# Kernel optimization log

Measured on AMD Instinct MI355X. Metric: run time of the kernel, lower is better.

## Reference

```python
import jax, jax.numpy as jnp
import numpy as np

NUM_STATION = 20
NUM_HEADS = 8
INPUT_DIM = 128
KEY_DIM = 16          # = val_dim = embed_dim // num_heads
EMBED_DIM = 128
NORM = 1.0 / np.sqrt(KEY_DIM).astype(np.float32)


def setup_inputs() -> dict:
    key = jax.random.key(0)
    ks = jax.random.split(key, 10)
    B, N, D = 32, 1024, INPUT_DIM
    q = jax.random.normal(ks[0], (B, N, D), jnp.float32)
    h = jax.random.normal(ks[1], (B, N, D), jnp.float32)
    stdv_k = 1.0 / np.sqrt(KEY_DIM)      # torch init: uniform(-1/sqrt(last_dim), ...)
    stdv_e = 1.0 / np.sqrt(EMBED_DIM)
    def U(k, shape, s):
        return jax.random.uniform(k, shape, jnp.float32, -s, s)
    pshape = (NUM_HEADS, INPUT_DIM, KEY_DIM)
    return {
        "q": q,
        "h": h,
        "W_query_custom": U(ks[2], pshape, stdv_k),
        "W_query_custom_1": U(ks[3], pshape, stdv_k),
        "W_key_custom": U(ks[4], pshape, stdv_k),
        "W_val_custom": U(ks[5], pshape, stdv_k),
        "W_query_charge_1": U(ks[6], pshape, stdv_k),
        "W_key_charge": U(ks[7], pshape, stdv_k),
        "W_val_charge": U(ks[8], pshape, stdv_k),
        "W_out": U(ks[9], (NUM_HEADS, KEY_DIM, EMBED_DIM), stdv_e),
    }


def reference(q, h, W_query_custom, W_query_custom_1, W_key_custom, W_val_custom,
              W_query_charge_1, W_key_charge, W_val_charge, W_out):
    S = NUM_STATION + 1                      # depot + stations
    h_st, h_tk = h[:, :S], h[:, S:]          # [B,S,D], [B,T,D]
    q_st, q_tk = q[:, :S], q[:, S:]

    proj = lambda x, W: jnp.einsum('bnd,hdk->hbnk', x, W)

    K_c = proj(h_tk, W_key_custom)           # [H,B,T,K]
    V_c = proj(h_tk, W_val_custom)
    K_s = proj(h_st, W_key_charge)           # [H,B,S,K]
    V_s = proj(h_st, W_val_charge)

    # task -> task attention (queries via W_query_custom_1)
    Q_tt = proj(q_tk, W_query_custom_1)
    A_tt = jax.nn.softmax(NORM * jnp.einsum('hbqk,hbtk->hbqt', Q_tt, K_c), axis=-1)
    heads_t = jnp.einsum('hbqt,hbtk->hbqk', A_tt, V_c)

    # task -> station attention (queries via W_query_custom)
    Q_ts = proj(q_tk, W_query_custom)
    A_ts = jax.nn.softmax(NORM * jnp.einsum('hbqk,hbsk->hbqs', Q_ts, K_s), axis=-1)
    heads_t = heads_t + jnp.einsum('hbqs,hbsk->hbqk', A_ts, V_s)

    # station -> task attention (queries via W_query_charge_1)
    Q_st = proj(q_st, W_query_charge_1)
    A_st = jax.nn.softmax(NORM * jnp.einsum('hbqk,hbtk->hbqt', Q_st, K_c), axis=-1)
    heads_s = jnp.einsum('hbqt,hbtk->hbqk', A_st, V_c)

    heads = jnp.concatenate([heads_s, heads_t], axis=2)   # [H,B,N,K]
    out = jnp.einsum('hbnk,hke->bne', heads, W_out)        # [B,N,E]
    return out
```

## Files before the change

kernel.cpp:

```cpp
#include <hip/hip_runtime.h>

typedef __bf16 bf16x8 __attribute__((ext_vector_type(8)));
typedef float f32x4 __attribute__((ext_vector_type(4)));
typedef float f32x16 __attribute__((ext_vector_type(16)));
typedef unsigned int uint32;
typedef unsigned short u16;

#define NST 21
#define TOK 1003
#define SCL 0.3606737602222409f

union U4B { uint4 u; bf16x8 b; };

__device__ __forceinline__ uint32 pkbf(float a, float b) {
  uint32 ua = __float_as_uint(a), ub = __float_as_uint(b);
  ua += 0x7fffu + ((ua >> 16) & 1u);
  ub += 0x7fffu + ((ub >> 16) & 1u);
  return (ua >> 16) | (ub & 0xffff0000u);
}
__device__ __forceinline__ u16 bf1(float a) {
  uint32 u = __float_as_uint(a);
  u += 0x7fffu + ((u >> 16) & 1u);
  return (u16)(u >> 16);
}
__device__ __forceinline__ uint32 pkperm(float lo, float hi) {
  return __builtin_amdgcn_perm(__float_as_uint(hi), __float_as_uint(lo), 0x07060302u);
}
__device__ __forceinline__ void plswap(uint32& a, uint32& b) {
#if __has_builtin(__builtin_amdgcn_permlane32_swap)
  typedef unsigned int uu2 __attribute__((ext_vector_type(2)));
  uu2 r = __builtin_amdgcn_permlane32_swap(a, b, false, false);
  a = r.x; b = r.y;
#else
  asm volatile("v_permlane32_swap_b32 %0, %1" : "+v"(a), "+v"(b));
#endif
}

__global__ __launch_bounds__(256) void prep(
    const float* __restrict__ q, const float* __restrict__ hx,
    const float* __restrict__ W0, const float* __restrict__ W1,
    const float* __restrict__ W2, const float* __restrict__ W3,
    const float* __restrict__ W4, const float* __restrict__ Wqst,
    const float* __restrict__ Wks, const float* __restrict__ Wvs,
    u16* __restrict__ WtAll, u16* __restrict__ Qm,
    u16* __restrict__ Ks, u16* __restrict__ Vs) {
  int bid = blockIdx.x, tid = threadIdx.x;
  __shared__ float xq2[2][128], xh2[2][128];
  if (bid < 40) {
    int w = bid >> 3, seg = bid & 7;
    const float* W = (w == 0) ? W0 : (w == 1) ? W1 : (w == 2) ? W2
                     : (w == 3) ? W3 : W4;
    u16* dst = WtAll + w * 16384;
#pragma unroll
    for (int it = 0; it < 8; ++it) {
      int i = seg * 2048 + it * 256 + tid;
      int inner = i & 127, outer = i >> 7;
      float v;
      if (w < 4) {
        int h = outer >> 4, k = outer & 15;
        v = W[h * 2048 + inner * 16 + k];
      } else {
        v = W[inner * 128 + outer];
      }
      dst[outer * 128 + inner] = bf1(v);
    }
  } else {
    int t2 = bid - 40;
    int sub = tid >> 7, col = tid & 127;
    int hh = col >> 4, k = col & 15;
    int bs2 = t2 * 2 + sub;
    int b2 = bs2 >> 5, s = bs2 & 31;
    if (s < NST) {
      xq2[sub][col] = q[(size_t)(b2 * 1024 + s) * 128 + col];
      xh2[sub][col] = hx[(size_t)(b2 * 1024 + s) * 128 + col];
    }
    __syncthreads();
    if (s < NST) {
      const float* Wq = Wqst + hh * 2048 + k;
      const float* Wk = Wks + hh * 2048 + k;
      const float* Wv = Wvs + hh * 2048 + k;
      float dq = 0.f, dk_ = 0.f, dv = 0.f;
#pragma unroll 8
      for (int d = 0; d < 128; ++d) {
        float xq = xq2[sub][d], xh = xh2[sub][d];
        dq = fmaf(xq, Wq[d * 16], dq);
        dk_ = fmaf(xh, Wk[d * 16], dk_);
        dv = fmaf(xh, Wv[d * 16], dv);
      }
      Qm[(((size_t)hh * 32 + b2) * 1024 + s) * 16 + k] = bf1(dq * SCL);
      Ks[(((size_t)hh * 32 + b2) * 32 + s) * 16 + k] = bf1(dk_);
      Vs[(((size_t)hh * 32 + b2) * 16 + k) * 32 + s] = bf1(dv);
    } else {
      Ks[(((size_t)hh * 32 + b2) * 32 + s) * 16 + k] = 0;
      Vs[(((size_t)hh * 32 + b2) * 16 + k) * 32 + s] = 0;
    }
  }
}

__global__ __launch_bounds__(256) void proj_pair(
    const float* __restrict__ q, const float* __restrict__ hx,
    const u16* __restrict__ WtAll, u16* __restrict__ Qm,
    u16* __restrict__ Qts, u16* __restrict__ Kc, u16* __restrict__ Vc) {
  __shared__ u16 Wl[128 * 136];
  int pg = blockIdx.x >> 9, mb = blockIdx.x & 511;
  int m0 = mb * 64;
  const float* A = pg ? hx : q;
  int tid = threadIdx.x;
  int wave = tid >> 6, lane = tid & 63;
  int quad = lane >> 4, l15 = lane & 15;
  int mrow = m0 + wave * 16 + l15;

  U4B af[4];
#pragma unroll
  for (int dk = 0; dk < 4; ++dk) {
    const float* Af = A + (size_t)mrow * 128 + dk * 32 + quad * 8;
    float4 a = *(const float4*)Af;
    float4 b = *(const float4*)(Af + 4);
    af[dk].u = make_uint4(pkbf(a.x, a.y), pkbf(a.z, a.w),
                          pkbf(b.x, b.y), pkbf(b.z, b.w));
  }

  int gbase = m0 + wave * 16 + quad * 4;
  int bb = gbase >> 10, n0 = gbase & 1023;
  int token = mrow;
  int bb2 = token >> 10, tn = token & 1023;

#pragma unroll
  for (int s = 0; s < 2; ++s) {
    int mode = pg * 2 + s;
    const u16* WtG = WtAll + mode * 16384;
    if (s) __syncthreads();
#pragma unroll
    for (int r = 0; r < 8; ++r) {
      int i = r * 256 + tid;
      int e = i >> 4, j = i & 15;
      *(uint4*)&Wl[e * 136 + j * 8] = *(const uint4*)(WtG + e * 128 + j * 8);
    }
    __syncthreads();

    f32x4 c[8];
#pragma unroll
    for (int nt = 0; nt < 8; ++nt)
#pragma unroll
      for (int r = 0; r < 4; ++r) c[nt][r] = 0.f;
#pragma unroll
    for (int dk = 0; dk < 4; ++dk)
#pragma unroll
      for (int nt = 0; nt < 8; ++nt) {
        U4B bg;
        bg.u = *(const uint4*)&Wl[(nt * 16 + l15) * 136 + dk * 32 + quad * 8];
        if (mode == 3)
          c[nt] = __builtin_amdgcn_mfma_f32_16x16x32_bf16(af[dk].b, bg.b, c[nt], 0, 0, 0);
        else
          c[nt] = __builtin_amdgcn_mfma_f32_16x16x32_bf16(bg.b, af[dk].b, c[nt], 0, 0, 0);
      }

    if (mode == 3) {
#pragma unroll
      for (int nt = 0; nt < 8; ++nt) {
        uint2 w2 = make_uint2(pkbf(c[nt][0], c[nt][1]), pkbf(c[nt][2], c[nt][3]));
        *(uint2*)(Vc + (((size_t)nt * 32 + bb) * 16 + l15) * 1024 + n0) = w2;
      }
    } else {
      float scale = (mode <= 1) ? SCL : 1.0f;
      u16* dstp = (mode == 0) ? Qm : (mode == 1) ? Qts : Kc;
      if (mode != 0 || tn >= NST) {
#pragma unroll
        for (int nt = 0; nt < 8; ++nt) {
          uint2 w2 = make_uint2(pkbf(c[nt][0] * scale, c[nt][1] * scale),
                                pkbf(c[nt][2] * scale, c[nt][3] * scale));
          *(uint2*)(dstp + (((size_t)nt * 32 + bb2) * 1024 + tn) * 16 + quad * 4) = w2;
        }
      }
    }
  }
}

__global__ __launch_bounds__(256) void outproj(
    const u16* __restrict__ heads, const u16* __restrict__ WtAll,
    float* __restrict__ out) {
  __shared__ u16 Wl[128 * 136];
  const u16* WtG = WtAll + 4 * 16384;
  int tid = threadIdx.x;
#pragma unroll
  for (int r = 0; r < 8; ++r) {
    int i = r * 256 + tid;
    int e = i >> 4, j = i & 15;
    *(uint4*)&Wl[e * 136 + j * 8] = *(const uint4*)(WtG + e * 128 + j * 8);
  }
  __syncthreads();
  int wave = tid >> 6, lane = tid & 63;
  int quad = lane >> 4, l15 = lane & 15;
  int m0 = blockIdx.x * 64;
  int mrow = m0 + wave * 16 + l15;

  f32x4 c[8];
#pragma unroll
  for (int nt = 0; nt < 8; ++nt)
#pragma unroll
    for (int r = 0; r < 4; ++r) c[nt][r] = 0.f;
#pragma unroll
  for (int dk = 0; dk < 4; ++dk) {
    U4B af;
    af.u = *(const uint4*)(heads + (size_t)mrow * 128 + dk * 32 + quad * 8);
#pragma unroll
    for (int nt = 0; nt < 8; ++nt) {
      U4B bg;
      bg.u = *(const uint4*)&Wl[(nt * 16 + l15) * 136 + dk * 32 + quad * 8];
      c[nt] = __builtin_amdgcn_mfma_f32_16x16x32_bf16(bg.b, af.b, c[nt], 0, 0, 0);
    }
  }
#pragma unroll
  for (int nt = 0; nt < 8; ++nt)
    *(f32x4*)(out + (size_t)mrow * 128 + nt * 16 + quad * 4) = c[nt];
}

__global__ __launch_bounds__(256, 6) void attn_main(
    const u16* __restrict__ Qm, const u16* __restrict__ Qts,
    const u16* __restrict__ Kc, const u16* __restrict__ Vc,
    const u16* __restrict__ Ks, const u16* __restrict__ Vs,
    u16* __restrict__ heads) {
  int bx = blockIdx.x;
  int hb = bx & 255, qc = bx >> 8;
  int h = hb >> 5, b = hb & 31;
  int tid = threadIdx.x;
  int wave = tid >> 6, lane = tid & 63;
  int l5 = lane >> 5, l31 = lane & 31;

  __shared__ u16 Kl[128 * 26];
  __shared__ u16 Vl[32 * 140];
  __shared__ u16 KsL[32 * 26];
  __shared__ u16 VsL[32 * 44];

  const u16* Qbase = Qm + ((size_t)(h * 32 + b)) * 16384;
  const u16* QtsB = Qts + ((size_t)(h * 32 + b)) * 16384;
  const u16* Kbase = Kc + ((size_t)(h * 32 + b)) * 16384;
  const u16* Vbase = Vc + ((size_t)(h * 32 + b)) * 16384;
  const u16* KsB = Ks + (size_t)(h * 32 + b) * 512;
  const u16* VsB = Vs + (size_t)(h * 32 + b) * 512;

  uint4 ones4 = make_uint4(0x3F803F80u, 0x3F803F80u, 0x3F803F80u, 0x3F803F80u);

  if (tid < 64) {
    int key = tid >> 1, half = tid & 1;
    *(uint4*)&KsL[key * 26 + half * 8] = *(const uint4*)(KsB + key * 16 + half * 8);
  } else if (tid < 128) {
    int t = tid - 64;
    int d = t >> 2, kg = t & 3;
    *(uint4*)&VsL[d * 44 + kg * 8] = *(const uint4*)(VsB + d * 32 + kg * 8);
  } else if (tid < 192) {
    int t = tid - 128;
    *(uint4*)&VsL[(16 + (t >> 2)) * 44 + (t & 3) * 8] = ones4;
  }
  *(uint4*)&Vl[(16 + (tid >> 4)) * 140 + (tid & 15) * 8] = ones4;

  int skey = tid >> 1, shalf = tid & 1;
  int sd = tid >> 4, skg = tid & 15;
  uint4 kpre = *(const uint4*)(Kbase + (size_t)skey * 16 + shalf * 8);
  uint4 vpre = *(const uint4*)(Vbase + (size_t)sd * 1024 + skg * 8);

  int qw0 = qc * 128 + wave * 32;
  int qrow = qw0 + l31;

  f32x16 zero16;
#pragma unroll
  for (int i = 0; i < 16; ++i) zero16[i] = 0.f;

  U4B qf;
  qf.u = *(const uint4*)(QtsB + (size_t)qrow * 16 + l5 * 8);
  __syncthreads();
  float contrib[8];
  {
    U4B af;
    af.u = *(const uint4*)&KsL[l31 * 26 + l5 * 8];
    f32x16 c0 =
        __builtin_amdgcn_mfma_f32_32x32x16_bf16(af.b, qf.b, zero16, 0, 0, 0);
    uint32 w[8];
#pragma unroll
    for (int g = 0; g < 4; ++g) {
      float p0 = __builtin_amdgcn_exp2f(c0[4 * g + 0]);
      float p1 = __builtin_amdgcn_exp2f(c0[4 * g + 1]);
      float p2 = __builtin_amdgcn_exp2f(c0[4 * g + 2]);
      float p3 = __builtin_amdgcn_exp2f(c0[4 * g + 3]);
      int kb0 = 8 * g + 4 * l5;
      p0 = (kb0 + 0 >= NST) ? 0.f : p0;
      p1 = (kb0 + 1 >= NST) ? 0.f : p1;
      p2 = (kb0 + 2 >= NST) ? 0.f : p2;
      p3 = (kb0 + 3 >= NST) ? 0.f : p3;
      w[2 * g] = pkperm(p0, p1);
      w[2 * g + 1] = pkperm(p2, p3);
    }
    plswap(w[0], w[2]); plswap(w[1], w[3]);
    plswap(w[4], w[6]); plswap(w[5], w[7]);
    U4B b1, b2, a1, a2;
    b1.u = make_uint4(w[0], w[1], w[2], w[3]);
    b2.u = make_uint4(w[4], w[5], w[6], w[7]);
    a1.u = *(const uint4*)&VsL[l31 * 44 + l5 * 8];
    a2.u = *(const uint4*)&VsL[l31 * 44 + 16 + l5 * 8];
    f32x16 acc2 =
        __builtin_amdgcn_mfma_f32_32x32x16_bf16(a1.b, b1.b, zero16, 0, 0, 0);
    acc2 = __builtin_amdgcn_mfma_f32_32x32x16_bf16(a2.b, b2.b, acc2, 0, 0, 0);
    float rla2 = __builtin_amdgcn_rcpf(acc2[8]);
#pragma unroll
    for (int r = 0; r < 8; ++r) contrib[r] = acc2[r] * rla2;
  }

  qf.u = *(const uint4*)(Qbase + (size_t)qrow * 16 + l5 * 8);
  f32x16 acc;
#pragma unroll
  for (int i = 0; i < 16; ++i) acc[i] = 0.f;

#pragma unroll 1
  for (int kb = 0; kb < 8; ++kb) {
    __syncthreads();
    *(uint4*)&Kl[skey * 26 + shalf * 8] = kpre;
    *(uint4*)&Vl[sd * 140 + skg * 8] = vpre;
    if (kb < 7) {
      int j0n = (kb + 1) * 128;
      kpre = *(const uint4*)(Kbase + (size_t)(j0n + skey) * 16 + shalf * 8);
      vpre = *(const uint4*)(Vbase + (size_t)sd * 1024 + j0n + skg * 8);
    }
    __syncthreads();

    U4B af0;
    af0.u = *(const uint4*)&Kl[l31 * 26 + l5 * 8];
    f32x16 c0 =
        __builtin_amdgcn_mfma_f32_32x32x16_bf16(af0.b, qf.b, zero16, 0, 0, 0);
#pragma unroll
    for (int kt = 0; kt < 4; ++kt) {
      f32x16 cn;
      if (kt < 3) {
        U4B afn;
        afn.u = *(const uint4*)&Kl[((kt + 1) * 32 + l31) * 26 + l5 * 8];
        cn = __builtin_amdgcn_mfma_f32_32x32x16_bf16(afn.b, qf.b, zero16, 0, 0, 0);
      }
      int key0 = kt * 32;
      bool masked = (kb == 0) && (kt == 0);
      uint32 w[8];
#pragma unroll
      for (int g = 0; g < 4; ++g) {
        float p0 = __builtin_amdgcn_exp2f(c0[4 * g + 0]);
        float p1 = __builtin_amdgcn_exp2f(c0[4 * g + 1]);
        float p2 = __builtin_amdgcn_exp2f(c0[4 * g + 2]);
        float p3 = __builtin_amdgcn_exp2f(c0[4 * g + 3]);
        if (masked) {
          int kb0 = 8 * g + 4 * l5;
          p0 = (kb0 + 0 < NST) ? 0.f : p0;
          p1 = (kb0 + 1 < NST) ? 0.f : p1;
          p2 = (kb0 + 2 < NST) ? 0.f : p2;
          p3 = (kb0 + 3 < NST) ? 0.f : p3;
        }
        w[2 * g] = pkperm(p0, p1);
        w[2 * g + 1] = pkperm(p2, p3);
      }
      plswap(w[0], w[2]); plswap(w[1], w[3]);
      plswap(w[4], w[6]); plswap(w[5], w[7]);
      U4B b1, b2, a1, a2;
      b1.u = make_uint4(w[0], w[1], w[2], w[3]);
      b2.u = make_uint4(w[4], w[5], w[6], w[7]);
      a1.u = *(const uint4*)&Vl[l31 * 140 + key0 + l5 * 8];
      a2.u = *(const uint4*)&Vl[l31 * 140 + key0 + 16 + l5 * 8];
      acc = __builtin_amdgcn_mfma_f32_32x32x16_bf16(a1.b, b1.b, acc, 0, 0, 0);
      acc = __builtin_amdgcn_mfma_f32_32x32x16_bf16(a2.b, b2.b, acc, 0, 0, 0);
      if (kt < 3) c0 = cn;
    }
  }

  {
    float rla = __builtin_amdgcn_rcpf(acc[8]);
    bool tok = (qrow >= NST);
    float v0 = acc[0] * rla + (tok ? contrib[0] : 0.f);
    float v1 = acc[1] * rla + (tok ? contrib[1] : 0.f);
    float v2 = acc[2] * rla + (tok ? contrib[2] : 0.f);
    float v3 = acc[3] * rla + (tok ? contrib[3] : 0.f);
    float v4 = acc[4] * rla + (tok ? contrib[4] : 0.f);
    float v5 = acc[5] * rla + (tok ? contrib[5] : 0.f);
    float v6 = acc[6] * rla + (tok ? contrib[6] : 0.f);
    float v7 = acc[7] * rla + (tok ? contrib[7] : 0.f);
    u16* hrow = heads + ((size_t)b * 1024 + qrow) * 128 + h * 16;
    *(uint2*)(hrow + 4 * l5) = make_uint2(pkbf(v0, v1), pkbf(v2, v3));
    *(uint2*)(hrow + 8 + 4 * l5) = make_uint2(pkbf(v4, v5), pkbf(v6, v7));
  }
}

extern "C" void kernel_launch(void* const* d_in, const int* in_sizes, int n_in,
                              void* d_out, int out_size, void* d_ws,
                              size_t ws_size, hipStream_t stream) {
  (void)in_sizes; (void)n_in; (void)out_size; (void)ws_size;
  const float* q     = (const float*)d_in[0];
  const float* hx    = (const float*)d_in[1];
  const float* W_qts = (const float*)d_in[2];
  const float* W_qtt = (const float*)d_in[3];
  const float* W_kc  = (const float*)d_in[4];
  const float* W_vc  = (const float*)d_in[5];
  const float* W_qst = (const float*)d_in[6];
  const float* W_ks  = (const float*)d_in[7];
  const float* W_vs  = (const float*)d_in[8];
  const float* W_out = (const float*)d_in[9];

  char* ws = (char*)d_ws;
  u16* heads = (u16*)(ws + 0);
  u16* Qm    = (u16*)(ws + 16777216);
  u16* Qts   = (u16*)(ws + 25165824);
  u16* Kc    = (u16*)(ws + 33554432);
  u16* Vc    = (u16*)(ws + 41943040);
  u16* Ks    = (u16*)(ws + 50331648);
  u16* Vs    = (u16*)(ws + 50593792);
  u16* WtAll = (u16*)(ws + 50855936);

  hipLaunchKernelGGL(prep, dim3(552), dim3(256), 0, stream,
                     q, hx, W_qtt, W_qts, W_kc, W_vc, W_out, W_qst, W_ks, W_vs,
                     WtAll, Qm, Ks, Vs);
  hipLaunchKernelGGL(proj_pair, dim3(1024), dim3(256), 0, stream,
                     q, hx, WtAll, Qm, Qts, Kc, Vc);
  hipLaunchKernelGGL(attn_main, dim3(2048), dim3(256), 0, stream,
                     Qm, Qts, Kc, Vc, Ks, Vs, heads);
  hipLaunchKernelGGL(outproj, dim3(512), dim3(256), 0, stream,
                     heads, WtAll, (float*)d_out);
}
```

Baseline: 164.9 us.

## Double-buffer K/V tiles in LDS, shrink V buffers, relayout heads head-major

The attention loop now double-buffers K and V tiles in shared memory, so each iteration needs one barrier instead of two. The ones-rows used for the softmax denominator are supplied from registers rather than stored in LDS, which roughly halves the V buffer footprint. Occupancy hint rises from 6 to 8 blocks, and s_setprio wraps the PV MFMAs. The heads intermediate is written head-major, and the output projection reads it from that layout, which gives more contiguous stores but more strided loads in the projection kernel.

After: 165.9 us. No clear change (+0.6%).

```diff
diff --git a/kernel.cpp b/kernel.cpp
--- a/kernel.cpp
+++ b/kernel.cpp
@@ -202,7 +202,9 @@
 #pragma unroll
   for (int dk = 0; dk < 4; ++dk) {
     U4B af;
-    af.u = *(const uint4*)(heads + (size_t)mrow * 128 + dk * 32 + quad * 8);
+    int h2 = dk * 2 + (quad >> 1);
+    int k0 = (quad & 1) * 8;
+    af.u = *(const uint4*)(heads + ((size_t)h2 * 32768 + mrow) * 16 + k0);
 #pragma unroll
     for (int nt = 0; nt < 8; ++nt) {
       U4B bg;
@@ -215,7 +217,7 @@
     *(f32x4*)(out + (size_t)mrow * 128 + nt * 16 + quad * 4) = c[nt];
 }
 
-__global__ __launch_bounds__(256, 6) void attn_main(
+__global__ __launch_bounds__(256, 8) void attn_main(
     const u16* __restrict__ Qm, const u16* __restrict__ Qts,
     const u16* __restrict__ Kc, const u16* __restrict__ Vc,
     const u16* __restrict__ Ks, const u16* __restrict__ Vs,
@@ -227,10 +229,10 @@
   int wave = tid >> 6, lane = tid & 63;
   int l5 = lane >> 5, l31 = lane & 31;
 
-  __shared__ u16 Kl[128 * 26];
-  __shared__ u16 Vl[32 * 140];
+  __shared__ u16 Kl[2][128 * 26];
+  __shared__ u16 Vl[2][16 * 140];
   __shared__ u16 KsL[32 * 26];
-  __shared__ u16 VsL[32 * 44];
+  __shared__ u16 VsL[16 * 44];
 
   const u16* Qbase = Qm + ((size_t)(h * 32 + b)) * 16384;
   const u16* QtsB = Qts + ((size_t)(h * 32 + b)) * 16384;
@@ -248,11 +250,7 @@
     int t = tid - 64;
     int d = t >> 2, kg = t & 3;
     *(uint4*)&VsL[d * 44 + kg * 8] = *(const uint4*)(VsB + d * 32 + kg * 8);
-  } else if (tid < 192) {
-    int t = tid - 128;
-    *(uint4*)&VsL[(16 + (t >> 2)) * 44 + (t & 3) * 8] = ones4;
-  }
-  *(uint4*)&Vl[(16 + (tid >> 4)) * 140 + (tid & 15) * 8] = ones4;
+  }
 
   int skey = tid >> 1, shalf = tid & 1;
   int sd = tid >> 4, skg = tid & 15;
@@ -268,7 +266,14 @@
 
   U4B qf;
   qf.u = *(const uint4*)(QtsB + (size_t)qrow * 16 + l5 * 8);
+
+  *(uint4*)&Kl[0][skey * 26 + shalf * 8] = kpre;
+  *(uint4*)&Vl[0][sd * 140 + skg * 8] = vpre;
+  kpre = *(const uint4*)(Kbase + (size_t)(128 + skey) * 16 + shalf * 8);
+  vpre = *(const uint4*)(Vbase + (size_t)sd * 1024 + 128 + skg * 8);
+
   __syncthreads();
+
   float contrib[8];
   {
     U4B af;
@@ -295,8 +300,11 @@
     U4B b1, b2, a1, a2;
     b1.u = make_uint4(w[0], w[1], w[2], w[3]);
     b2.u = make_uint4(w[4], w[5], w[6], w[7]);
-    a1.u = *(const uint4*)&VsL[l31 * 44 + l5 * 8];
-    a2.u = *(const uint4*)&VsL[l31 * 44 + 16 + l5 * 8];
+    a1.u = ones4; a2.u = ones4;
+    if (l31 < 16) {
+      a1.u = *(const uint4*)&VsL[l31 * 44 + l5 * 8];
+      a2.u = *(const uint4*)&VsL[l31 * 44 + 16 + l5 * 8];
+    }
     f32x16 acc2 =
         __builtin_amdgcn_mfma_f32_32x32x16_bf16(a1.b, b1.b, zero16, 0, 0, 0);
     acc2 = __builtin_amdgcn_mfma_f32_32x32x16_bf16(a2.b, b2.b, acc2, 0, 0, 0);
@@ -312,18 +320,18 @@
 
 #pragma unroll 1
   for (int kb = 0; kb < 8; ++kb) {
-    __syncthreads();
-    *(uint4*)&Kl[skey * 26 + shalf * 8] = kpre;
-    *(uint4*)&Vl[sd * 140 + skg * 8] = vpre;
+    int cb = kb & 1;
     if (kb < 7) {
-      int j0n = (kb + 1) * 128;
-      kpre = *(const uint4*)(Kbase + (size_t)(j0n + skey) * 16 + shalf * 8);
-      vpre = *(const uint4*)(Vbase + (size_t)sd * 1024 + j0n + skg * 8);
-    }
-    __syncthreads();
-
+      *(uint4*)&Kl[cb ^ 1][skey * 26 + shalf * 8] = kpre;
+      *(uint4*)&Vl[cb ^ 1][sd * 140 + skg * 8] = vpre;
+      if (kb < 6) {
+        int j0n = (kb + 2) * 128;
+        kpre = *(const uint4*)(Kbase + (size_t)(j0n + skey) * 16 + shalf * 8);
+        vpre = *(const uint4*)(Vbase + (size_t)sd * 1024 + j0n + skg * 8);
+      }
+    }
     U4B af0;
-    af0.u = *(const uint4*)&Kl[l31 * 26 + l5 * 8];
+    af0.u = *(const uint4*)&Kl[cb][l31 * 26 + l5 * 8];
     f32x16 c0 =
         __builtin_amdgcn_mfma_f32_32x32x16_bf16(af0.b, qf.b, zero16, 0, 0, 0);
 #pragma unroll
@@ -331,7 +339,7 @@
       f32x16 cn;
       if (kt < 3) {
         U4B afn;
-        afn.u = *(const uint4*)&Kl[((kt + 1) * 32 + l31) * 26 + l5 * 8];
+        afn.u = *(const uint4*)&Kl[cb][((kt + 1) * 32 + l31) * 26 + l5 * 8];
         cn = __builtin_amdgcn_mfma_f32_32x32x16_bf16(afn.b, qf.b, zero16, 0, 0, 0);
       }
       int key0 = kt * 32;
@@ -358,12 +366,18 @@
       U4B b1, b2, a1, a2;
       b1.u = make_uint4(w[0], w[1], w[2], w[3]);
       b2.u = make_uint4(w[4], w[5], w[6], w[7]);
-      a1.u = *(const uint4*)&Vl[l31 * 140 + key0 + l5 * 8];
-      a2.u = *(const uint4*)&Vl[l31 * 140 + key0 + 16 + l5 * 8];
+      a1.u = ones4; a2.u = ones4;
+      if (l31 < 16) {
+        a1.u = *(const uint4*)&Vl[cb][l31 * 140 + key0 + l5 * 8];
+        a2.u = *(const uint4*)&Vl[cb][l31 * 140 + key0 + 16 + l5 * 8];
+      }
+      __builtin_amdgcn_s_setprio(1);
       acc = __builtin_amdgcn_mfma_f32_32x32x16_bf16(a1.b, b1.b, acc, 0, 0, 0);
       acc = __builtin_amdgcn_mfma_f32_32x32x16_bf16(a2.b, b2.b, acc, 0, 0, 0);
+      __builtin_amdgcn_s_setprio(0);
       if (kt < 3) c0 = cn;
     }
+    __syncthreads();
   }
 
   {
@@ -377,7 +391,7 @@
     float v5 = acc[5] * rla + (tok ? contrib[5] : 0.f);
     float v6 = acc[6] * rla + (tok ? contrib[6] : 0.f);
     float v7 = acc[7] * rla + (tok ? contrib[7] : 0.f);
-    u16* hrow = heads + ((size_t)b * 1024 + qrow) * 128 + h * 16;
+    u16* hrow = heads + (((size_t)(h * 32 + b)) * 1024 + qrow) * 16;
     *(uint2*)(hrow + 4 * l5) = make_uint2(pkbf(v0, v1), pkbf(v2, v3));
     *(uint2*)(hrow + 8 + 4 * l5) = make_uint2(pkbf(v4, v5), pkbf(v6, v7));
   }
```
